# Kernel tuning notes

Hardware: AMD Instinct MI355X
Metric: run time of the kernel (lower is better)

Reference implementation:

```python
import jax, jax.numpy as jnp
import numpy as np

BETA_INIT = 0.9
THRESHOLD = 1.0
SLOPE = 4.0  # surrogate sigmoid slope


def setup_inputs() -> dict:
    key = jax.random.key(0)
    k1, k2, k3 = jax.random.split(key, 3)
    B, S, D, F = 2, 2048, 1024, 4096
    x = jax.random.normal(k1, (B, S, D), dtype=jnp.float32)
    w_up = jax.random.normal(k2, (F, D), dtype=jnp.float32) / np.sqrt(D)
    w_down = jax.random.normal(k3, (D, F), dtype=jnp.float32) / np.sqrt(F)
    beta = jnp.full((F,), BETA_INIT, dtype=jnp.float32)
    return {"x": x, "w_up": w_up, "w_down": w_down, "beta": beta, "T": 8}


def _spike(v):
    # Heaviside forward, sigmoid surrogate gradient (straight-through).
    surr = jax.nn.sigmoid(SLOPE * (v - THRESHOLD))
    hard = (v > THRESHOLD).astype(v.dtype)
    return surr + jax.lax.stop_gradient(hard - surr)


def reference(x, w_up, w_down, beta, T):
    # up-projection: [B,S,D] @ [F,D]^T -> [B,S,F]
    h = jnp.einsum('bsd,fd->bsf', x, w_up)

    def step(carry, _):
        v, ssum = carry
        v = beta * v + h                 # leaky integrate (same input each step)
        s = _spike(v)                    # fire
        v = v - s * THRESHOLD            # soft reset
        return (v, ssum + s), None

    v0 = jnp.zeros_like(h)
    (v_final, spike_sum), _ = jax.lax.scan(step, (v0, jnp.zeros_like(h)), None, length=T)
    rate = spike_sum / T                             # [B,S,F] mean spike rate
    rate_per_unit = jnp.mean(rate, axis=(0, 1))      # [F] per-unit firing rate
    out = jnp.einsum('bsf,df->bsd', rate, w_down)    # down-projection (dropout=0)
    return out, rate_per_unit
```

## Files before the change

kernel.cpp:

```cpp
#include <hip/hip_runtime.h>

#define N_ROWS 4096
#define DDIM   1024
#define FDIM   4096

typedef unsigned short u16;
typedef __attribute__((ext_vector_type(8))) _Float16 f16x8;
typedef __attribute__((ext_vector_type(4))) float f32x4;

#define MFMA16(a, b, c) __builtin_amdgcn_mfma_f32_16x16x32_f16((a), (b), (c), 0, 0, 0)

static __device__ __forceinline__ u16 f2h_bits(float f) {
    _Float16 h = (_Float16)f;
    return __builtin_bit_cast(u16, h);
}
static __device__ __forceinline__ void gload_lds16(const u16* g, u16* l) {
    __builtin_amdgcn_global_load_lds((const __attribute__((address_space(1))) unsigned*)g,
                                     (__attribute__((address_space(3))) unsigned*)l, 16, 0, 0);
}

__global__ __launch_bounds__(256) void split_all(
    const float* __restrict__ x, const float* __restrict__ wup,
    const float* __restrict__ wdown,
    u16* __restrict__ xh, u16* __restrict__ xl,
    u16* __restrict__ wh, u16* __restrict__ wd, float* __restrict__ colsum)
{
    const int N4 = (N_ROWS * DDIM) / 4;
    int i = blockIdx.x * 256 + threadIdx.x;
    if (i < FDIM / 4) ((float4*)colsum)[i] = (float4){0.f, 0.f, 0.f, 0.f};
    const int stride = gridDim.x * 256;
    for (; i < 3 * N4; i += stride) {
        const int r = i >> 20;
        const int j = i & (N4 - 1);
        if (r == 0) {
            float4 v = ((const float4*)x)[j];
            ushort4 h, l;
            h.x = f2h_bits(v.x); h.y = f2h_bits(v.y);
            h.z = f2h_bits(v.z); h.w = f2h_bits(v.w);
            l.x = f2h_bits(v.x - (float)__builtin_bit_cast(_Float16, h.x));
            l.y = f2h_bits(v.y - (float)__builtin_bit_cast(_Float16, h.y));
            l.z = f2h_bits(v.z - (float)__builtin_bit_cast(_Float16, h.z));
            l.w = f2h_bits(v.w - (float)__builtin_bit_cast(_Float16, h.w));
            ((ushort4*)xh)[j] = h;
            ((ushort4*)xl)[j] = l;
        } else {
            const float4 v = (r == 1) ? ((const float4*)wup)[j] : ((const float4*)wdown)[j];
            ushort4 h;
            h.x = f2h_bits(v.x); h.y = f2h_bits(v.y);
            h.z = f2h_bits(v.z); h.w = f2h_bits(v.w);
            if (r == 1) ((ushort4*)wh)[j] = h; else ((ushort4*)wd)[j] = h;
        }
    }
}

__global__ __launch_bounds__(512, 1) void up_mfma(
    const u16* __restrict__ xh, const u16* __restrict__ xl,
    const u16* __restrict__ wh,
    const float* __restrict__ beta, const int* __restrict__ Tp,
    u16* __restrict__ rate, float* __restrict__ colsum)
{
    __shared__ __align__(16) u16 lds[3 * 24576];

    const int t = threadIdx.x;
    const int l = t & 63, w = t >> 6;
    const int wm = w >> 1, wn = w & 1;

    const int flat = blockIdx.y * gridDim.x + blockIdx.x;
    const int xcd = flat & 7, wi = flat >> 3;
    const int bm = ((xcd & 3) * 4 + (wi & 3)) * 256;
    const int bn = ((xcd >> 2) * 8 + (wi >> 2)) * 256;

    const int srow = t >> 2;
    const int koff = (((t & 3) ^ ((t >> 3) & 3)) << 3);
    const size_t gA0 = (size_t)(bm + srow) * DDIM + koff;
    const size_t gA1 = gA0 + (size_t)128 * DDIM;
    const size_t gB0 = (size_t)(bn + srow) * DDIM + koff;
    const size_t gB1 = gB0 + (size_t)128 * DDIM;
    const int dst = t * 8;

#define STG(slot, step) do {                                                  \
    const size_t k0_ = (size_t)(step) << 5;                                   \
    u16* Lb_ = &lds[(slot) * 24576];                                          \
    gload_lds16(xh + gA0 + k0_, Lb_ + dst);                                   \
    gload_lds16(xh + gA1 + k0_, Lb_ + 4096 + dst);                            \
    gload_lds16(xl + gA0 + k0_, Lb_ + 8192 + dst);                            \
    gload_lds16(xl + gA1 + k0_, Lb_ + 12288 + dst);                           \
    gload_lds16(wh + gB0 + k0_, Lb_ + 16384 + dst);                           \
    gload_lds16(wh + gB1 + k0_, Lb_ + 20480 + dst);                           \
} while (0)

    const int lr = l & 15, lk = l >> 4;
    const int psl = ((lk ^ ((lr >> 1) & 3)) << 3);

    f32x4 acc[4][8];
#pragma unroll
    for (int m = 0; m < 4; ++m)
#pragma unroll
        for (int n = 0; n < 8; ++n) acc[m][n] = (f32x4){0.f, 0.f, 0.f, 0.f};

    STG(0, 0);
    STG(1, 1);

    const int NT = DDIM / 32;
#pragma unroll 1
    for (int ts = 0; ts < NT; ++ts) {
        if (ts + 1 < NT) { asm volatile("s_waitcnt vmcnt(6)" ::: "memory"); }
        else             { asm volatile("s_waitcnt vmcnt(0)" ::: "memory"); }
        __builtin_amdgcn_s_barrier();

        if (ts + 2 < NT) STG((ts + 2) % 3, ts + 2);

        const int sb = (ts % 3) * 24576;
        f16x8 ah[4], al[4], bh[8];
#pragma unroll
        for (int m = 0; m < 4; ++m) {
            const int ro = sb + (wm * 64 + m * 16 + lr) * 32 + psl;
            ah[m] = *(const f16x8*)&lds[ro];
            al[m] = *(const f16x8*)&lds[ro + 8192];
        }
#pragma unroll
        for (int n = 0; n < 8; ++n) {
            const int ro = sb + 16384 + (wn * 128 + n * 16 + lr) * 32 + psl;
            bh[n] = *(const f16x8*)&lds[ro];
        }
        __builtin_amdgcn_s_setprio(1);
#pragma unroll
        for (int m = 0; m < 4; ++m)
#pragma unroll
            for (int n = 0; n < 8; ++n) {
                f32x4 c = acc[m][n];
                c = MFMA16(ah[m], bh[n], c);
                c = MFMA16(al[m], bh[n], c);
                acc[m][n] = c;
            }
        __builtin_amdgcn_s_setprio(0);
    }
#undef STG

    const int T = Tp[0];
    const float invT = 1.0f / (float)T;
    const int fbase = bn + wn * 128;
    float betav[8], colacc[8];
#pragma unroll
    for (int n = 0; n < 8; ++n) { betav[n] = beta[fbase + n * 16 + lr]; colacc[n] = 0.f; }

#pragma unroll
    for (int m = 0; m < 4; ++m) {
#pragma unroll
        for (int r = 0; r < 4; ++r) {
            const int row = bm + wm * 64 + m * 16 + lk * 4 + r;
            u16* rp = rate + (size_t)row * FDIM + fbase + lr;
#pragma unroll
            for (int n = 0; n < 8; ++n) {
                const float h = acc[m][n][r];
                const float bet = betav[n];
                float v = 0.f, ss = 0.f;
                if (T == 8) {
#pragma unroll
                    for (int tt = 0; tt < 8; ++tt) {
                        v = fmaf(bet, v, h);
                        float s = (v > 1.0f) ? 1.0f : 0.0f;
                        ss += s; v -= s;
                    }
                } else {
                    for (int tt = 0; tt < T; ++tt) {
                        v = fmaf(bet, v, h);
                        float s = (v > 1.0f) ? 1.0f : 0.0f;
                        ss += s; v -= s;
                    }
                }
                const float rv = ss * invT;
                rp[n * 16] = f2h_bits(rv);
                colacc[n] += rv;
            }
        }
    }
#pragma unroll
    for (int n = 0; n < 8; ++n) {
        float ca = colacc[n];
        ca += __shfl_xor(ca, 16, 64);
        ca += __shfl_xor(ca, 32, 64);
        if (lk == 0) atomicAdd(&colsum[fbase + n * 16 + lr], ca);
    }
}

__global__ __launch_bounds__(512, 1) void down_mfma(
    const u16* __restrict__ rate, const u16* __restrict__ wd,
    float* __restrict__ out)
{
    __shared__ __align__(16) u16 lds[3 * 16384];

    const int t = threadIdx.x;
    const int l = t & 63, w = t >> 6;
    const int wm = w >> 2, wn = w & 3;

    const int flat = blockIdx.y * gridDim.x + blockIdx.x;
    const int xcd = flat & 7, wi = flat >> 3;
    const int bm = ((xcd & 3) * 8 + (wi & 7)) * 128;
    const int bn = ((xcd >> 2) * 4 + (wi >> 3)) * 128;

    const int srow = t >> 3;
    const int koff = (((t & 7) ^ ((t >> 3) & 7)) << 3);
    const size_t gA0 = (size_t)(bm + srow) * FDIM + koff;
    const size_t gA1 = gA0 + (size_t)64 * FDIM;
    const size_t gB0 = (size_t)(bn + srow) * FDIM + koff;
    const size_t gB1 = gB0 + (size_t)64 * FDIM;
    const int dst = t * 8;

#define STD(slot, step) do {                                                  \
    const size_t k0_ = (size_t)(step) << 6;                                   \
    u16* Lb_ = &lds[(slot) * 16384];                                          \
    gload_lds16(rate + gA0 + k0_, Lb_ + dst);                                 \
    gload_lds16(rate + gA1 + k0_, Lb_ + 4096 + dst);                          \
    gload_lds16(wd + gB0 + k0_, Lb_ + 8192 + dst);                            \
    gload_lds16(wd + gB1 + k0_, Lb_ + 12288 + dst);                           \
} while (0)

    const int lr = l & 15, lk = l >> 4;
    const int key = lr & 7;
    const int ps0 = ((0 * 4 + lk) ^ key) << 3;
    const int ps1 = ((1 * 4 + lk) ^ key) << 3;

    f32x4 acc[4][2];
#pragma unroll
    for (int m = 0; m < 4; ++m) {
        acc[m][0] = (f32x4){0.f, 0.f, 0.f, 0.f};
        acc[m][1] = (f32x4){0.f, 0.f, 0.f, 0.f};
    }

    STD(0, 0);
    STD(1, 1);

    const int NT = FDIM / 64;
#pragma unroll 1
    for (int ts = 0; ts < NT; ++ts) {
        if (ts + 1 < NT) { asm volatile("s_waitcnt vmcnt(4)" ::: "memory"); }
        else             { asm volatile("s_waitcnt vmcnt(0)" ::: "memory"); }
        __builtin_amdgcn_s_barrier();

        if (ts + 2 < NT) STD((ts + 2) % 3, ts + 2);

        const int sb = (ts % 3) * 16384;
        f16x8 a[4][2], b[2][2];
#pragma unroll
        for (int m = 0; m < 4; ++m) {
            const int ro = sb + (wm * 64 + m * 16 + lr) * 64;
            a[m][0] = *(const f16x8*)&lds[ro + ps0];
            a[m][1] = *(const f16x8*)&lds[ro + ps1];
        }
#pragma unroll
        for (int n = 0; n < 2; ++n) {
            const int ro = sb + 8192 + (wn * 32 + n * 16 + lr) * 64;
            b[n][0] = *(const f16x8*)&lds[ro + ps0];
            b[n][1] = *(const f16x8*)&lds[ro + ps1];
        }
        __builtin_amdgcn_s_setprio(1);
#pragma unroll
        for (int m = 0; m < 4; ++m)
#pragma unroll
            for (int n = 0; n < 2; ++n) {
                f32x4 c = acc[m][n];
                c = MFMA16(a[m][0], b[n][0], c);
                c = MFMA16(a[m][1], b[n][1], c);
                acc[m][n] = c;
            }
        __builtin_amdgcn_s_setprio(0);
    }
#undef STD

#pragma unroll
    for (int n = 0; n < 2; ++n) {
        const int d = bn + wn * 32 + n * 16 + lr;
#pragma unroll
        for (int m = 0; m < 4; ++m) {
            const int row0 = bm + wm * 64 + m * 16 + lk * 4;
#pragma unroll
            for (int r = 0; r < 4; ++r)
                out[(size_t)(row0 + r) * DDIM + d] = acc[m][n][r];
        }
    }
}

__global__ void finalize_rpu(const float* __restrict__ colsum, float* __restrict__ out_rpu) {
    const int f = blockIdx.x * 256 + threadIdx.x;
    out_rpu[f] = colsum[f] * (1.0f / (float)N_ROWS);
}

extern "C" void kernel_launch(void* const* d_in, const int* in_sizes, int n_in,
                              void* d_out, int out_size, void* d_ws, size_t ws_size,
                              hipStream_t stream) {
    const float* x     = (const float*)d_in[0];
    const float* wup   = (const float*)d_in[1];
    const float* wdown = (const float*)d_in[2];
    const float* beta  = (const float*)d_in[3];
    const int*   Tp    = (const int*)d_in[4];

    float* out     = (float*)d_out;
    float* out_rpu = out + (size_t)N_ROWS * DDIM;

    char* ws = (char*)d_ws;
    u16* rate = (u16*)ws;
    u16* xh   = (u16*)(ws + 33554432);
    u16* xl   = (u16*)(ws + 33554432 + 8388608);
    u16* wh   = (u16*)(ws + 33554432 + 2 * 8388608);
    u16* wd   = (u16*)(ws + 33554432 + 3 * 8388608);
    float* colsum = (float*)(ws + 33554432 + 4 * 8388608);

    split_all<<<2048, 256, 0, stream>>>(x, wup, wdown, xh, xl, wh, wd, colsum);

    up_mfma<<<dim3(16, 16), 512, 0, stream>>>(xh, xl, wh, beta, Tp, rate, colsum);

    finalize_rpu<<<FDIM / 256, 256, 0, stream>>>(colsum, out_rpu);

    down_mfma<<<dim3(DDIM / 128, N_ROWS / 128), 512, 0, stream>>>(rate, wd, out);
}
```

Before: 147.3 us.

## Shrink up-proj tiles to 128x128, load x-low straight into registers

The up-projection kernel moves from 256x256 tiles with 512 threads to 128x128 tiles with 256 threads and up to three blocks per CU, which gives 1024 blocks instead of 256. The low-half x fragments no longer go through LDS. Each wave prefetches them from global memory straight into registers one k-step ahead, which shrinks LDS use and the stage traffic. The aim is better occupancy and latency hiding. The cost is less reuse per tile, since the A and B operands are reloaded more often from L2, plus direct global loads that are not coalesced through LDS.

```diff
diff --git a/kernel.cpp b/kernel.cpp
--- a/kernel.cpp
+++ b/kernel.cpp
@@ -53,13 +53,13 @@
     }
 }
 
-__global__ __launch_bounds__(512, 1) void up_mfma(
+__global__ __launch_bounds__(256, 3) void up_mfma(
     const u16* __restrict__ xh, const u16* __restrict__ xl,
     const u16* __restrict__ wh,
     const float* __restrict__ beta, const int* __restrict__ Tp,
     u16* __restrict__ rate, float* __restrict__ colsum)
 {
-    __shared__ __align__(16) u16 lds[3 * 24576];
+    __shared__ __align__(16) u16 lds[3 * 8192];
 
     const int t = threadIdx.x;
     const int l = t & 63, w = t >> 6;
@@ -67,70 +67,77 @@
 
     const int flat = blockIdx.y * gridDim.x + blockIdx.x;
     const int xcd = flat & 7, wi = flat >> 3;
-    const int bm = ((xcd & 3) * 4 + (wi & 3)) * 256;
-    const int bn = ((xcd >> 2) * 8 + (wi >> 2)) * 256;
-
-    const int srow = t >> 2;
+    const int bm = ((xcd & 3) * 8 + (wi & 7)) * 128;
+    const int bn = ((xcd >> 2) * 16 + (wi >> 3)) * 128;
+
     const int koff = (((t & 3) ^ ((t >> 3) & 3)) << 3);
-    const size_t gA0 = (size_t)(bm + srow) * DDIM + koff;
-    const size_t gA1 = gA0 + (size_t)128 * DDIM;
-    const size_t gB0 = (size_t)(bn + srow) * DDIM + koff;
-    const size_t gB1 = gB0 + (size_t)128 * DDIM;
+    const size_t gA0 = (size_t)(bm + (t >> 2)) * DDIM + koff;
+    const size_t gA1 = gA0 + (size_t)64 * DDIM;
+    const size_t gB0 = (size_t)(bn + (t >> 2)) * DDIM + koff;
+    const size_t gB1 = gB0 + (size_t)64 * DDIM;
     const int dst = t * 8;
 
 #define STG(slot, step) do {                                                  \
     const size_t k0_ = (size_t)(step) << 5;                                   \
-    u16* Lb_ = &lds[(slot) * 24576];                                          \
+    u16* Lb_ = &lds[(slot) * 8192];                                           \
     gload_lds16(xh + gA0 + k0_, Lb_ + dst);                                   \
-    gload_lds16(xh + gA1 + k0_, Lb_ + 4096 + dst);                            \
-    gload_lds16(xl + gA0 + k0_, Lb_ + 8192 + dst);                            \
-    gload_lds16(xl + gA1 + k0_, Lb_ + 12288 + dst);                           \
-    gload_lds16(wh + gB0 + k0_, Lb_ + 16384 + dst);                           \
-    gload_lds16(wh + gB1 + k0_, Lb_ + 20480 + dst);                           \
+    gload_lds16(xh + gA1 + k0_, Lb_ + 2048 + dst);                            \
+    gload_lds16(wh + gB0 + k0_, Lb_ + 4096 + dst);                            \
+    gload_lds16(wh + gB1 + k0_, Lb_ + 6144 + dst);                            \
 } while (0)
 
     const int lr = l & 15, lk = l >> 4;
     const int psl = ((lk ^ ((lr >> 1) & 3)) << 3);
 
-    f32x4 acc[4][8];
+    const u16* xlbase = xl + (size_t)(bm + wm * 64 + lr) * DDIM + lk * 8;
+
+    f32x4 acc[4][4];
 #pragma unroll
     for (int m = 0; m < 4; ++m)
 #pragma unroll
-        for (int n = 0; n < 8; ++n) acc[m][n] = (f32x4){0.f, 0.f, 0.f, 0.f};
-
+        for (int n = 0; n < 4; ++n) acc[m][n] = (f32x4){0.f, 0.f, 0.f, 0.f};
+
+    f16x8 cur[4], nxt[4];
+#pragma unroll
+    for (int m = 0; m < 4; ++m)
+        nxt[m] = *(const f16x8*)(xlbase + (size_t)(m * 16) * DDIM);
     STG(0, 0);
     STG(1, 1);
 
     const int NT = DDIM / 32;
 #pragma unroll 1
     for (int ts = 0; ts < NT; ++ts) {
-        if (ts + 1 < NT) { asm volatile("s_waitcnt vmcnt(6)" ::: "memory"); }
-        else             { asm volatile("s_waitcnt vmcnt(0)" ::: "memory"); }
+        if (ts == 0) { asm volatile("s_waitcnt vmcnt(4)" ::: "memory"); }
+        else         { asm volatile("s_waitcnt vmcnt(8)" ::: "memory"); }
         __builtin_amdgcn_s_barrier();
 
+#pragma unroll
+        for (int m = 0; m < 4; ++m) cur[m] = nxt[m];
+        if (ts + 1 < NT) {
+            const size_t ko = (size_t)((ts + 1) << 5);
+#pragma unroll
+            for (int m = 0; m < 4; ++m)
+                nxt[m] = *(const f16x8*)(xlbase + (size_t)(m * 16) * DDIM + ko);
+        }
         if (ts + 2 < NT) STG((ts + 2) % 3, ts + 2);
 
-        const int sb = (ts % 3) * 24576;
-        f16x8 ah[4], al[4], bh[8];
-#pragma unroll
-        for (int m = 0; m < 4; ++m) {
-            const int ro = sb + (wm * 64 + m * 16 + lr) * 32 + psl;
-            ah[m] = *(const f16x8*)&lds[ro];
-            al[m] = *(const f16x8*)&lds[ro + 8192];
-        }
-#pragma unroll
-        for (int n = 0; n < 8; ++n) {
-            const int ro = sb + 16384 + (wn * 128 + n * 16 + lr) * 32 + psl;
-            bh[n] = *(const f16x8*)&lds[ro];
-        }
+        const int sb = (ts % 3) * 8192;
+        f16x8 ah[4], b[4];
+#pragma unroll
+        for (int m = 0; m < 4; ++m)
+            ah[m] = *(const f16x8*)&lds[sb + (wm * 64 + m * 16 + lr) * 32 + psl];
+#pragma unroll
+        for (int n = 0; n < 4; ++n)
+            b[n] = *(const f16x8*)&lds[sb + 4096 + (wn * 64 + n * 16 + lr) * 32 + psl];
+
         __builtin_amdgcn_s_setprio(1);
 #pragma unroll
         for (int m = 0; m < 4; ++m)
 #pragma unroll
-            for (int n = 0; n < 8; ++n) {
+            for (int n = 0; n < 4; ++n) {
                 f32x4 c = acc[m][n];
-                c = MFMA16(ah[m], bh[n], c);
-                c = MFMA16(al[m], bh[n], c);
+                c = MFMA16(ah[m], b[n], c);
+                c = MFMA16(cur[m], b[n], c);
                 acc[m][n] = c;
             }
         __builtin_amdgcn_s_setprio(0);
@@ -139,10 +146,10 @@
 
     const int T = Tp[0];
     const float invT = 1.0f / (float)T;
-    const int fbase = bn + wn * 128;
-    float betav[8], colacc[8];
-#pragma unroll
-    for (int n = 0; n < 8; ++n) { betav[n] = beta[fbase + n * 16 + lr]; colacc[n] = 0.f; }
+    const int fbase = bn + wn * 64;
+    float betav[4], colacc[4];
+#pragma unroll
+    for (int n = 0; n < 4; ++n) { betav[n] = beta[fbase + n * 16 + lr]; colacc[n] = 0.f; }
 
 #pragma unroll
     for (int m = 0; m < 4; ++m) {
@@ -151,7 +158,7 @@
             const int row = bm + wm * 64 + m * 16 + lk * 4 + r;
             u16* rp = rate + (size_t)row * FDIM + fbase + lr;
 #pragma unroll
-            for (int n = 0; n < 8; ++n) {
+            for (int n = 0; n < 4; ++n) {
                 const float h = acc[m][n][r];
                 const float bet = betav[n];
                 float v = 0.f, ss = 0.f;
@@ -176,7 +183,7 @@
         }
     }
 #pragma unroll
-    for (int n = 0; n < 8; ++n) {
+    for (int n = 0; n < 4; ++n) {
         float ca = colacc[n];
         ca += __shfl_xor(ca, 16, 64);
         ca += __shfl_xor(ca, 32, 64);
@@ -308,7 +315,7 @@
 
     split_all<<<2048, 256, 0, stream>>>(x, wup, wdown, xh, xl, wh, wd, colsum);
 
-    up_mfma<<<dim3(16, 16), 512, 0, stream>>>(xh, xl, wh, beta, Tp, rate, colsum);
+    up_mfma<<<dim3(32, 32), 256, 0, stream>>>(xh, xl, wh, beta, Tp, rate, colsum);
 
     finalize_rpu<<<FDIM / 256, 256, 0, stream>>>(colsum, out_rpu);
 
```

Result: slower. 161.1 us (+9.4%).
